# Performance work log

Measured on AMD Instinct MI355X. Metric: run time of the kernel, lower is better.

Reference implementation:

```python
import jax, jax.numpy as jnp
import numpy as np

B, N, F, T, K, C, CT = 64, 307, 64, 12, 3, 64, 64
LN_EPS = 1e-5


def setup_inputs() -> dict:
    key = jax.random.key(0)
    ks = jax.random.split(key, 20)
    s = 0.1  # mild scale so sigmoid/softmax stay in a sane range
    return {
        "x": jax.random.normal(ks[0], (B, N, F, T), jnp.float32),
        "W1": jax.random.normal(ks[1], (T,), jnp.float32) * s,
        "W2": jax.random.normal(ks[2], (F, T), jnp.float32) * s,
        "W3": jax.random.normal(ks[3], (F,), jnp.float32) * s,
        "b_s": jax.random.normal(ks[4], (1, N, N), jnp.float32) * s,
        "V_s": jax.random.normal(ks[5], (N, N), jnp.float32) * s,
        "U1": jax.random.normal(ks[6], (N,), jnp.float32) * s,
        "U2": jax.random.normal(ks[7], (F, N), jnp.float32) * s,
        "U3": jax.random.normal(ks[8], (F,), jnp.float32) * s,
        "b_e": jax.random.normal(ks[9], (1, T, T), jnp.float32) * s,
        "V_e": jax.random.normal(ks[10], (T, T), jnp.float32) * s,
        "cheb": jax.random.normal(ks[11], (K, N, N), jnp.float32) * s,
        "Theta": jax.random.normal(ks[12], (K, F, C), jnp.float32) * s,
        "tconv_w": jax.random.normal(ks[13], (CT, C, 1, 3), jnp.float32) * s,
        "tconv_b": jax.random.normal(ks[14], (CT,), jnp.float32) * s,
        "rconv_w": jax.random.normal(ks[15], (CT, F, 1, 1), jnp.float32) * s,
        "rconv_b": jax.random.normal(ks[16], (CT,), jnp.float32) * s,
        "gamma": jnp.ones((CT,), jnp.float32),
        "beta": jnp.zeros((CT,), jnp.float32),
    }


def _temporal_attention(x, U1, U2, U3, b_e, V_e):
    # x: (B,N,F,T)
    lhs = jnp.einsum('bnft,n->btf', x, U1) @ U2            # (B,T,N)
    rhs = jnp.einsum('f,bnft->bnt', U3, x)                 # (B,N,T)
    prod = jnp.einsum('btn,bns->bts', lhs, rhs)            # (B,T,T)
    E = jnp.einsum('uv,bvt->but', V_e, jax.nn.sigmoid(prod + b_e))
    return jax.nn.softmax(E, axis=1)                       # (B,T,T)


def _spatial_attention(x, W1, W2, W3, b_s, V_s):
    # x: (B,N,F,T)
    lhs = jnp.einsum('bnft,t->bnf', x, W1) @ W2            # (B,N,T)
    rhs = jnp.einsum('f,bnft->btn', W3, x)                 # (B,T,N)
    prod = jnp.einsum('bnt,btm->bnm', lhs, rhs)            # (B,N,N)
    sig = jax.nn.sigmoid(prod + b_s)                       # (B,N,N)
    # torch: (V_s @ sig.T(1,2,0)).T(2,0,1) -> S[b,a,i] = sum_v V_s[i,v]*sig[b,a,v]
    S = jnp.einsum('bav,iv->bai', sig, V_s)
    return jax.nn.softmax(S, axis=1)                       # (B,N,N)


def _cheb_conv_sat(x, S, cheb, Theta):
    # x: (B,N,F,T), S: (B,N,N), cheb: (K,N,N), Theta: (K,F,C)
    A = cheb[:, None] * S[None]                            # (K,B,N,N) attention-masked polys
    # out[b,j,c,t] = sum_{k,i,f} A[k,b,i,j] * x[b,i,f,t] * Theta[k,f,c]
    rhs = jnp.einsum('kbij,bift->kbjft', A, x)             # (K,B,N,F,T)
    out = jnp.einsum('kbjft,kfc->bjct', rhs, Theta)        # (B,N,C,T)
    return jax.nn.relu(out)


def _conv2d(inp, w, b, pad):
    # inp: (B,C_in,N,T), w: (C_out,C_in,kh,kw)
    y = jax.lax.conv_general_dilated(
        inp, w, window_strides=(1, 1), padding=pad,
        dimension_numbers=('NCHW', 'OIHW', 'NCHW'))
    return y + b[None, :, None, None]


def reference(x, W1, W2, W3, b_s, V_s, U1, U2, U3, b_e, V_e,
              cheb, Theta, tconv_w, tconv_b, rconv_w, rconv_b, gamma, beta):
    b, n, f_, t = x.shape
    # temporal attention gating
    E = _temporal_attention(x, U1, U2, U3, b_e, V_e)                      # (B,T,T)
    x_TAt = (x.reshape(b, n * f_, t) @ E).reshape(b, n, f_, t)
    # spatial attention on temporally-gated signal
    S = _spatial_attention(x_TAt, W1, W2, W3, b_s, V_s)                   # (B,N,N)
    # attention-weighted Chebyshev graph conv on original x
    spatial_gcn = _cheb_conv_sat(x, S, cheb, Theta)                       # (B,N,C,T)
    # temporal conv (1,3), SAME padding along time
    tco = _conv2d(spatial_gcn.transpose(0, 2, 1, 3), tconv_w, tconv_b,
                  ((0, 0), (1, 1))).transpose(0, 2, 1, 3)                 # (B,N,CT,T)
    # 1x1 residual conv on x
    res = _conv2d(x.transpose(0, 2, 1, 3), rconv_w, rconv_b,
                  ((0, 0), (0, 0))).transpose(0, 2, 1, 3)                 # (B,N,CT,T)
    h = jax.nn.relu(res + tco)
    # LayerNorm over the filter/channel axis (axis=2)
    mu = jnp.mean(h, axis=2, keepdims=True)
    var = jnp.var(h, axis=2, keepdims=True)
    hn = (h - mu) * jax.lax.rsqrt(var + LN_EPS)
    return hn * gamma[None, None, :, None] + beta[None, None, :, None]
```

## Files before the change

### kernel.cpp

```cpp
#include <hip/hip_runtime.h>
#include <hip/hip_bf16.h>
#include <math.h>

constexpr int B = 64, N = 307, F = 64, T = 12, K = 3, C = 64, CT = 64;
constexpr float LN_EPS = 1e-5f;
constexpr int FT = F * T;

typedef float vf4 __attribute__((ext_vector_type(4)));
typedef short s16x8 __attribute__((ext_vector_type(8)));

__device__ __forceinline__ unsigned short f2bf(float f) {
    unsigned int u = __float_as_uint(f);
    unsigned int r = u + 0x7FFFu + ((u >> 16) & 1u);
    return (unsigned short)(r >> 16);
}


__global__ void k_lhs1_e(const float* __restrict__ x, const float* __restrict__ U1,
                         float* __restrict__ out) {
    int bb = blockIdx.x;
    int b = bb / 3;
    int e = (bb % 3) * 256 + threadIdx.x;
    const float* xp = x + (size_t)b * N * FT + e;
    float s = 0.f;
    for (int n = 0; n < N; n++) s += xp[(size_t)n * FT] * U1[n];
    int f = e / T, t = e % T;
    out[((size_t)b * T + t) * F + f] = s;
}

__global__ void k_xdots(const float* __restrict__ x, const float* __restrict__ U3,
                        const float* __restrict__ W3, float* __restrict__ rhs_e,
                        float* __restrict__ xw3) {
    int idx = blockIdx.x * blockDim.x + threadIdx.x;
    if (idx >= B * N * T) return;
    int t = idx % T;
    size_t bn = idx / T;
    const float* xp = x + bn * F * T + t;
    float s1 = 0.f, s2 = 0.f;
    for (int f = 0; f < F; f++) {
        float v = xp[f * T];
        s1 += U3[f] * v;
        s2 += W3[f] * v;
    }
    rhs_e[idx] = s1;
    xw3[idx] = s2;
}

__global__ void k_lhs_e(const float* __restrict__ lhs1, const float* __restrict__ U2,
                        float* __restrict__ out) {
    int idx = blockIdx.x * blockDim.x + threadIdx.x;
    if (idx >= B * T * N) return;
    int n = idx % N;
    int bt = idx / N;
    const float* lp = lhs1 + (size_t)bt * F;
    float s = 0.f;
    for (int f = 0; f < F; f++) s += lp[f] * U2[f * N + n];
    out[idx] = s;
}

__global__ void k_tatt(const float* __restrict__ lhs, const float* __restrict__ rhs,
                       const float* __restrict__ b_e, const float* __restrict__ V_e,
                       const float* __restrict__ W1, float* __restrict__ E,
                       float* __restrict__ EW1) {
    int b = blockIdx.x;
    int tid = threadIdx.x;
    __shared__ float ll[T][N + 1];
    __shared__ float rr_[T][N + 1];
    __shared__ float sig[T * T];
    __shared__ float Ev[T * T];
    __shared__ float mx[T], sm[T];
    for (int l = tid; l < T * N; l += 256) ll[l / N][l % N] = lhs[(size_t)b * T * N + l];
    for (int l = tid; l < N * T; l += 256) rr_[l % T][l / T] = rhs[(size_t)b * N * T + l];
    __syncthreads();
    if (tid < T * T) {
        int t = tid % T, u = tid / T;
        const vf4* lp4 = (const vf4*)&ll[u][0];
        const vf4* rp4 = (const vf4*)&rr_[t][0];
        float s = 0.f;
#pragma unroll 4
        for (int q = 0; q < 76; q++) {
            vf4 a = lp4[q], c = rp4[q];
            s += a[0] * c[0] + a[1] * c[1] + a[2] * c[2] + a[3] * c[3];
        }
        for (int n = 304; n < N; n++) s += ll[u][n] * rr_[t][n];
        s += b_e[u * T + t];
        sig[tid] = 1.f / (1.f + expf(-s));
    }
    __syncthreads();
    if (tid < T * T) {
        int t = tid % T, u = tid / T;
        float e = 0.f;
        for (int v = 0; v < T; v++) e += V_e[u * T + v] * sig[v * T + t];
        Ev[tid] = e;
    }
    __syncthreads();
    if (tid < T) {
        float m = -1e30f;
        for (int u = 0; u < T; u++) m = fmaxf(m, Ev[u * T + tid]);
        float s = 0.f;
        for (int u = 0; u < T; u++) s += expf(Ev[u * T + tid] - m);
        mx[tid] = m;
        sm[tid] = s;
    }
    __syncthreads();
    if (tid < T * T) {
        int t = tid % T;
        float val = expf(Ev[tid] - mx[t]) / sm[t];
        E[(size_t)b * T * T + tid] = val;
        sig[tid] = val;
    }
    __syncthreads();
    if (tid < T) {
        float s = 0.f;
        for (int t = 0; t < T; t++) s += sig[tid * T + t] * W1[t];
        EW1[(size_t)b * T + tid] = s;
    }
}


__global__ void k_lhs_sf(const float* __restrict__ x, const float* __restrict__ EW1,
                         const float* __restrict__ W2, float* __restrict__ lhs_s) {
    int blk = blockIdx.x;
    int sub = threadIdx.x >> 6;
    int ft = threadIdx.x & 63;
    size_t bn = (size_t)blk * 4 + sub;
    int b = (int)(bn / N);
    __shared__ float a[4][F];
    __shared__ float ew[4][T];
    if (ft < T) ew[sub][ft] = EW1[(size_t)b * T + ft];
    __syncthreads();
    const float* xp = x + bn * FT + ft * T;
    float s = 0.f;
#pragma unroll
    for (int tp = 0; tp < T; tp++) s += xp[tp] * ew[sub][tp];
    a[sub][ft] = s;
    __syncthreads();
    if (ft < T) {
        float s2 = 0.f;
#pragma unroll 8
        for (int f = 0; f < F; f++) s2 += a[sub][f] * W2[f * T + ft];
        lhs_s[bn * T + ft] = s2;
    }
}

__global__ void k_rhs_s2(const float* __restrict__ xw3, const float* __restrict__ E,
                         float* __restrict__ out) {
    int idx = blockIdx.x * blockDim.x + threadIdx.x;
    if (idx >= B * T * N) return;
    int m = idx % N;
    int t = (idx / N) % T;
    int b = idx / (N * T);
    const float* xp = xw3 + ((size_t)b * N + m) * T;
    const float* Ep = E + (size_t)b * T * T + t;
    float s = 0.f;
    for (int tp = 0; tp < T; tp++) s += xp[tp] * Ep[tp * T];
    out[idx] = s;
}

constexpr int PREP_NN = N * N;
constexpr int PREP_TW = CT * C * 3;
constexpr int PREP_TH = K * F * C;
constexpr int PREP_TOT = PREP_NN + PREP_TW + PREP_TH;
constexpr int PREP_CHT = K * N * N;
constexpr int PREP_TOT2 = PREP_TOT + PREP_CHT;

__global__ void k_prep(const float* __restrict__ V, const float* __restrict__ tw,
                       const float* __restrict__ Th, const float* __restrict__ cheb,
                       float* __restrict__ VT, float* __restrict__ twT,
                       float* __restrict__ ThT, float* __restrict__ chebT) {
    int idx = blockIdx.x * blockDim.x + threadIdx.x;
    if (idx < PREP_NN) {
        int v = idx % N;
        int i = idx / N;
        VT[(size_t)v * N + i] = V[(size_t)i * N + v];
    } else if (idx < PREP_NN + PREP_TW) {
        int l = idx - PREP_NN;
        int dt = l % 3;
        int c = (l / 3) % C;
        int ct = l / (3 * C);
        twT[((size_t)dt * CT + ct) * C + c] = tw[l];
    } else if (idx < PREP_TOT) {
        int l = idx - PREP_NN - PREP_TW;
        int c = l % C;
        int f = (l / C) % F;
        int k = l / (C * F);
        ThT[((size_t)k * C + c) * F + f] = Th[l];
    } else if (idx < PREP_TOT2) {
        int l = idx - PREP_TOT;
        int i = l % N;
        int j = (l / N) % N;
        int k = l / (N * N);
        chebT[((size_t)k * N + j) * N + i] = cheb[((size_t)k * N + i) * N + j];
    }
}

constexpr int AT = 4;
constexpr int NAB = (N + AT - 1) / AT;

__global__ void k_sigS(const float* __restrict__ lhs_s, const float* __restrict__ rhs_s,
                       const float* __restrict__ b_s, const float* __restrict__ VsT,
                       float* __restrict__ S) {
    int blk = blockIdx.x;
    int b = blk / NAB;
    int a0 = (blk % NAB) * AT;
    int tid = threadIdx.x;
    __shared__ float lrow[AT][T];
    __shared__ float sig4[AT][N];
    if (tid < AT * T) {
        int a = tid / T, t = tid % T;
        lrow[a][t] = (a0 + a < N) ? lhs_s[((size_t)b * N + a0 + a) * T + t] : 0.f;
    }
    __syncthreads();
    for (int v = tid; v < N; v += 256) {
        float rv[T];
        for (int t = 0; t < T; t++) rv[t] = rhs_s[((size_t)b * T + t) * N + v];
        for (int a = 0; a < AT; a++) {
            if (a0 + a >= N) break;
            float s = 0.f;
            for (int t = 0; t < T; t++) s += lrow[a][t] * rv[t];
            s += b_s[(size_t)(a0 + a) * N + v];
            sig4[a][v] = 1.f / (1.f + expf(-s));
        }
    }
    __syncthreads();
    for (int i = tid; i < N; i += 256) {
        float s[AT] = {0.f, 0.f, 0.f, 0.f};
        for (int v = 0; v < N; v++) {
            float vt = VsT[(size_t)v * N + i];
            for (int a = 0; a < AT; a++) s[a] += sig4[a][v] * vt;
        }
        for (int a = 0; a < AT; a++)
            if (a0 + a < N) S[((size_t)b * N + a0 + a) * N + i] = s[a];
    }
}

__global__ void k_softmax_S(float* __restrict__ S) {
    int idx = blockIdx.x * blockDim.x + threadIdx.x;
    if (idx >= B * N) return;
    int b = idx / N;
    int i = idx % N;
    float* p = S + (size_t)b * N * N + i;
    float m = -1e30f;
    for (int a = 0; a < N; a++) m = fmaxf(m, p[(size_t)a * N]);
    float s = 0.f;
    for (int a = 0; a < N; a++) s += expf(p[(size_t)a * N] - m);
    float inv = 1.f / s;
    for (int a = 0; a < N; a++) p[(size_t)a * N] = expf(p[(size_t)a * N] - m) * inv;
}

__global__ void k_softT(const float* __restrict__ S, float* __restrict__ ST) {
    int b = blockIdx.x >> 1;
    int c0 = (blockIdx.x & 1) * 256;
    int tid = threadIdx.x;
    int c = c0 + tid;
    bool act = c < N;
    const float* p = S + (size_t)b * N * N + c;
    float m = -1e30f, s = 0.f;
    if (act) {
        for (int r = 0; r < N; r++) m = fmaxf(m, p[(size_t)r * N]);
        for (int r = 0; r < N; r++) s += expf(p[(size_t)r * N] - m);
    }
    float inv = act ? 1.f / s : 0.f;
    __shared__ float tile[32][257];
    float* STb = ST + (size_t)b * N * N;
    for (int r0 = 0; r0 < N; r0 += 32) {
        int rmax = min(32, N - r0);
        if (act)
            for (int rr = 0; rr < rmax; rr++)
                tile[rr][tid] = expf(p[(size_t)(r0 + rr) * N] - m) * inv;
        __syncthreads();
        for (int it = 0; it < 32; it++) {
            int cl = 8 * it + (tid >> 5);
            int cc = c0 + cl;
            int r = r0 + (tid & 31);
            if (cc < N && (tid & 31) < rmax) STb[(size_t)cc * N + r] = tile[tid & 31][cl];
        }
        __syncthreads();
    }
}


constexpr int JT = 4;
constexpr int NJB = (N + JT - 1) / JT;
constexpr int GGRID = B * NJB;
constexpr int IP = 320;

constexpr long XI_TOT = (long)B * 48 * 10 * 64;

__global__ void k_xI(const float* __restrict__ x, unsigned short* __restrict__ xI) {
    long idx = (long)blockIdx.x * 256 + threadIdx.x;
    if (idx >= XI_TOT) return;
    int lane = (int)(idx & 63);
    int ks = (int)((idx >> 6) % 10);
    int et = (int)((idx / 640) % 48);
    int b = (int)(idx / 30720);
    int col = lane & 15, kg = lane >> 4;
    int i0 = ks * 32 + kg * 8;
    int e = et * 16 + col;
    const float* xp = x + (size_t)b * N * FT + e;
    s16x8 out;
#pragma unroll
    for (int r = 0; r < 8; r++) {
        int i = i0 + r;
        out[r] = (i < N) ? (short)f2bf(xp[(size_t)i * FT]) : (short)0;
    }
    *(s16x8*)(xI + (size_t)idx * 8) = out;
}

__global__ void k_Wq16(const float* __restrict__ chebT, const float* __restrict__ ST,
                       unsigned short* __restrict__ Wq) {
    long idx = (long)blockIdx.x * 256 + threadIdx.x;
    long tot = (long)B * NJB * 12 * IP;
    if (idx >= tot) return;
    int i = (int)(idx % IP);
    int q = (int)((idx / IP) % 12);
    int jb = (int)((idx / (12L * IP)) % NJB);
    int b = (int)(idx / (12L * IP * NJB));
    int k = q >> 2, jj = q & 3, j = jb * 4 + jj;
    float w = 0.f;
    if (i < N && j < N)
        w = chebT[((size_t)k * N + j) * N + i] * ST[((size_t)b * N + j) * N + i];
    Wq[idx] = f2bf(w);
}

__global__ __launch_bounds__(256, 3) void k_gcnz_m(const unsigned short* __restrict__ xI,
                                                   const unsigned short* __restrict__ WqT,
                                                   const float* __restrict__ ThT,
                                                   float* __restrict__ sg) {
    int blk0 = blockIdx.x;
    int blk = (blk0 & 7) * (GGRID / 8) + (blk0 >> 3);
    int b = blk / NJB;
    int jb = blk % NJB;
    int j0 = jb * JT;
    int tid = threadIdx.x;
    int w = tid >> 6;
    int lane = tid & 63;
    int col = lane & 15;
    int kg = lane >> 4;

    __shared__ float zlf[3 * 3080];

    vf4 acc[12];
#pragma unroll
    for (int mt = 0; mt < 12; mt++) acc[mt] = (vf4){0.f, 0.f, 0.f, 0.f};

    const unsigned short* xb =
        xI + ((size_t)(b * 48 + w * 12) * 10) * 512 + (size_t)lane * 8;
    const unsigned short* wb =
        WqT + ((size_t)(b * NJB + jb) * 12 + (col < 12 ? col : 11)) * IP + kg * 8;

    s16x8 cx[6], nx[6], cw, nw;
    auto ldx = [&](s16x8* d, int h, int ks) {
#pragma unroll
        for (int m = 0; m < 6; m++)
            d[m] = *(const s16x8*)(xb + (size_t)((h * 6 + m) * 10 + ks) * 512);
    };

    cw = *(const s16x8*)(wb);
    ldx(cx, 0, 0);
#pragma unroll
    for (int step = 0; step < 20; step++) {
        int ks = step >> 1, h = step & 1;
        if (step < 19) {
            int ns = step + 1;
            int nks = ns >> 1, nh = ns & 1;
            nw = (nh == 0) ? *(const s16x8*)(wb + nks * 32) : cw;
            ldx(nx, nh, nks);
        }
#pragma unroll
        for (int m = 0; m < 6; m++)
            acc[h * 6 + m] =
                __builtin_amdgcn_mfma_f32_16x16x32_bf16(cw, cx[m], acc[h * 6 + m], 0, 0, 0);
        if (step < 19) {
            cw = nw;
#pragma unroll
            for (int m = 0; m < 6; m++) cx[m] = nx[m];
        }
        (void)ks;
    }

    if (kg < 3) {
#pragma unroll
        for (int mt = 0; mt < 12; mt++) {
            int e = w * 192 + mt * 16 + col;
            *(vf4*)(zlf + kg * 3080 + e * 4) = acc[mt];
        }
    }
    __syncthreads();

    if (tid < 192) {
        int t = tid % T;
        int c0 = (tid / T) * 4;
        float s[4][4];
#pragma unroll
        for (int cc = 0; cc < 4; cc++)
#pragma unroll
            for (int jj = 0; jj < 4; jj++) s[cc][jj] = 0.f;

#pragma unroll
        for (int k = 0; k < K; k++) {
            const vf4* zpk = (const vf4*)(zlf + k * 3080 + t * 4);
            const vf4* tp0 = (const vf4*)(ThT + ((size_t)k * C + c0 + 0) * F);
            const vf4* tp1 = (const vf4*)(ThT + ((size_t)k * C + c0 + 1) * F);
            const vf4* tp2 = (const vf4*)(ThT + ((size_t)k * C + c0 + 2) * F);
            const vf4* tp3 = (const vf4*)(ThT + ((size_t)k * C + c0 + 3) * F);
#pragma unroll 4
            for (int fq = 0; fq < F / 4; fq++) {
                vf4 z0 = zpk[(4 * fq + 0) * 12];
                vf4 z1 = zpk[(4 * fq + 1) * 12];
                vf4 z2 = zpk[(4 * fq + 2) * 12];
                vf4 z3 = zpk[(4 * fq + 3) * 12];
                vf4 th[4];
                th[0] = tp0[fq];
                th[1] = tp1[fq];
                th[2] = tp2[fq];
                th[3] = tp3[fq];
#pragma unroll
                for (int cc = 0; cc < 4; cc++) {
#pragma unroll
                    for (int jj = 0; jj < 4; jj++)
                        s[cc][jj] += th[cc][0] * z0[jj] + th[cc][1] * z1[jj] +
                                     th[cc][2] * z2[jj] + th[cc][3] * z3[jj];
                }
            }
        }
#pragma unroll
        for (int jj = 0; jj < 4; jj++) {
            int j = j0 + jj;
            if (j < N) {
                float* op = sg + ((size_t)b * N + j) * FT + (size_t)c0 * T + t;
                op[0 * T] = fmaxf(s[0][jj], 0.f);
                op[1 * T] = fmaxf(s[1][jj], 0.f);
                op[2 * T] = fmaxf(s[2][jj], 0.f);
                op[3 * T] = fmaxf(s[3][jj], 0.f);
            }
        }
    }
}


__global__ void k_Wp(const float* __restrict__ cheb, const float* __restrict__ S,
                     float* __restrict__ Wp) {
    long idx = (long)blockIdx.x * 256 + threadIdx.x;
    long tot = (long)B * NJB * N * 12;
    if (idx >= tot) return;
    int q = (int)(idx % 12);
    int i = (int)((idx / 12) % N);
    int jb = (int)((idx / (12L * N)) % NJB);
    int b = (int)(idx / (12L * N * NJB));
    int k = q >> 2, jj = q & 3;
    int j = jb * 4 + jj;
    float w = 0.f;
    if (j < N) w = cheb[((size_t)k * N + i) * N + j] * S[((size_t)b * N + i) * N + j];
    Wp[idx] = w;
}

__global__ __launch_bounds__(256, 4) void k_gcnz_p(const float* __restrict__ x,
                                                   const float* __restrict__ Wp,
                                                   const float* __restrict__ ThT,
                                                   float* __restrict__ sg) {
    int blk0 = blockIdx.x;
    int blk = (blk0 & 7) * (GGRID / 8) + (blk0 >> 3);
    int b = blk / NJB;
    int jb = blk % NJB;
    int j0 = jb * JT;
    int tid = threadIdx.x;

    __shared__ float zl[K][F][T][JT];

    float acc[K * JT][3];
#pragma unroll
    for (int m = 0; m < K * JT; m++)
#pragma unroll
        for (int r = 0; r < 3; r++) acc[m][r] = 0.f;

    const float* xp = x + (size_t)b * N * FT + 3 * tid;
    const float* wb = Wp + ((size_t)b * NJB + jb) * N * 12;

    float w0[12], w1[12], w2[12];
    float x0[3], x1[3], x2[3];

    auto LD = [&](float* wreg, float* xreg, int i) {
        const vf4* p = (const vf4*)(wb + (size_t)i * 12);
        vf4 a = p[0], b4 = p[1], c4 = p[2];
#pragma unroll
        for (int q = 0; q < 4; q++) {
            wreg[q] = a[q];
            wreg[4 + q] = b4[q];
            wreg[8 + q] = c4[q];
        }
        const float* xq = xp + (size_t)i * FT;
        xreg[0] = xq[0];
        xreg[1] = xq[1];
        xreg[2] = xq[2];
    };
    auto FMA = [&](const float* wreg, const float* xreg) {
#pragma unroll
        for (int m = 0; m < K * JT; m++) {
            acc[m][0] += wreg[m] * xreg[0];
            acc[m][1] += wreg[m] * xreg[1];
            acc[m][2] += wreg[m] * xreg[2];
        }
    };

    LD(w0, x0, 0);
    LD(w1, x1, 1);
    LD(w2, x2, 2);
    int i = 0;
    for (; i + 5 < N; i += 3) {
        float a0[12], a1[12], a2[12], y0[3], y1[3], y2[3];
        LD(a0, y0, i + 3);
        LD(a1, y1, i + 4);
        LD(a2, y2, i + 5);
        FMA(w0, x0);
        FMA(w1, x1);
        FMA(w2, x2);
#pragma unroll
        for (int m = 0; m < 12; m++) {
            w0[m] = a0[m];
            w1[m] = a1[m];
            w2[m] = a2[m];
        }
#pragma unroll
        for (int r = 0; r < 3; r++) {
            x0[r] = y0[r];
            x1[r] = y1[r];
            x2[r] = y2[r];
        }
    }
    FMA(w0, x0);
    FMA(w1, x1);
    FMA(w2, x2);
    for (i += 3; i < N; i++) {
        LD(w0, x0, i);
        FMA(w0, x0);
    }

#pragma unroll
    for (int r = 0; r < 3; r++) {
        int e = 3 * tid + r;
        int f = e / T, t = e % T;
#pragma unroll
        for (int m = 0; m < K * JT; m++) zl[m >> 2][f][t][m & 3] = acc[m][r];
    }
    __syncthreads();

    if (tid < 192) {
        int t = tid % T;
        int c0 = (tid / T) * 4;
        float s[4][4];
#pragma unroll
        for (int cc = 0; cc < 4; cc++)
#pragma unroll
            for (int jj = 0; jj < 4; jj++) s[cc][jj] = 0.f;

#pragma unroll
        for (int k = 0; k < K; k++) {
            const vf4* zpk = (const vf4*)&zl[k][0][t][0];
            const vf4* tp0 = (const vf4*)(ThT + ((size_t)k * C + c0 + 0) * F);
            const vf4* tp1 = (const vf4*)(ThT + ((size_t)k * C + c0 + 1) * F);
            const vf4* tp2 = (const vf4*)(ThT + ((size_t)k * C + c0 + 2) * F);
            const vf4* tp3 = (const vf4*)(ThT + ((size_t)k * C + c0 + 3) * F);
#pragma unroll 4
            for (int fq = 0; fq < F / 4; fq++) {
                vf4 z0 = zpk[(4 * fq + 0) * 12];
                vf4 z1 = zpk[(4 * fq + 1) * 12];
                vf4 z2 = zpk[(4 * fq + 2) * 12];
                vf4 z3 = zpk[(4 * fq + 3) * 12];
                vf4 th[4];
                th[0] = tp0[fq];
                th[1] = tp1[fq];
                th[2] = tp2[fq];
                th[3] = tp3[fq];
#pragma unroll
                for (int cc = 0; cc < 4; cc++) {
#pragma unroll
                    for (int jj = 0; jj < 4; jj++)
                        s[cc][jj] += th[cc][0] * z0[jj] + th[cc][1] * z1[jj] +
                                     th[cc][2] * z2[jj] + th[cc][3] * z3[jj];
                }
            }
        }
#pragma unroll
        for (int jj = 0; jj < 4; jj++) {
            int j = j0 + jj;
            if (j < N) {
                float* op = sg + ((size_t)b * N + j) * FT + (size_t)c0 * T + t;
                op[0 * T] = fmaxf(s[0][jj], 0.f);
                op[1 * T] = fmaxf(s[1][jj], 0.f);
                op[2 * T] = fmaxf(s[2][jj], 0.f);
                op[3 * T] = fmaxf(s[3][jj], 0.f);
            }
        }
    }
}


constexpr int RB = 4;
constexpr int PF = 68;

__global__ void k_rest(const float* __restrict__ x, const float* __restrict__ twT,
                       const float* __restrict__ tb, const float* __restrict__ rw,
                       const float* __restrict__ rb, const float* __restrict__ gamma,
                       const float* __restrict__ beta, float* __restrict__ io) {
    int blk = blockIdx.x;
    size_t bn0 = (size_t)blk * RB;
    int tid = threadIdx.x;

    __shared__ float xt[RB][T][PF];
    __shared__ float sgt[RB][T + 2][PF];
    __shared__ float red0[RB][T][17];
    __shared__ float red1[RB][T][17];
    __shared__ float mus[RB][T], rstds[RB][T];

    for (int l = tid; l < RB * PF; l += 192) {
        int rr = l / PF, c = l % PF;
        sgt[rr][0][c] = 0.f;
        sgt[rr][T + 1][c] = 0.f;
    }
    for (int l = tid; l < RB * FT; l += 192) {
        int rr = l / FT, rem = l % FT;
        int f = rem / T, t = rem % T;
        xt[rr][t][f] = x[(bn0 + rr) * FT + rem];
        sgt[rr][t + 1][f] = io[(bn0 + rr) * FT + rem];
    }
    __syncthreads();

    int t = tid % T;
    int cg = tid / T;
    int ct0 = cg * 4;

    float acc[RB][4];
#pragma unroll
    for (int rr = 0; rr < RB; rr++)
#pragma unroll
        for (int q = 0; q < 4; q++) acc[rr][q] = rb[ct0 + q] + tb[ct0 + q];

    {
        const vf4* w0 = (const vf4*)(rw + (size_t)(ct0 + 0) * F);
        const vf4* w1 = (const vf4*)(rw + (size_t)(ct0 + 1) * F);
        const vf4* w2 = (const vf4*)(rw + (size_t)(ct0 + 2) * F);
        const vf4* w3 = (const vf4*)(rw + (size_t)(ct0 + 3) * F);
#pragma unroll 4
        for (int fq = 0; fq < F / 4; fq++) {
            vf4 a = w0[fq], b4 = w1[fq], c4 = w2[fq], d4 = w3[fq];
#pragma unroll
            for (int rr = 0; rr < RB; rr++) {
                vf4 v = *(const vf4*)(&xt[rr][t][fq * 4]);
                acc[rr][0] += a[0] * v[0] + a[1] * v[1] + a[2] * v[2] + a[3] * v[3];
                acc[rr][1] += b4[0] * v[0] + b4[1] * v[1] + b4[2] * v[2] + b4[3] * v[3];
                acc[rr][2] += c4[0] * v[0] + c4[1] * v[1] + c4[2] * v[2] + c4[3] * v[3];
                acc[rr][3] += d4[0] * v[0] + d4[1] * v[1] + d4[2] * v[2] + d4[3] * v[3];
            }
        }
    }
#pragma unroll
    for (int dt = 0; dt < 3; dt++) {
        const vf4* w0 = (const vf4*)(twT + ((size_t)dt * CT + ct0 + 0) * C);
        const vf4* w1 = (const vf4*)(twT + ((size_t)dt * CT + ct0 + 1) * C);
        const vf4* w2 = (const vf4*)(twT + ((size_t)dt * CT + ct0 + 2) * C);
        const vf4* w3 = (const vf4*)(twT + ((size_t)dt * CT + ct0 + 3) * C);
#pragma unroll 4
        for (int fq = 0; fq < C / 4; fq++) {
            vf4 a = w0[fq], b4 = w1[fq], c4 = w2[fq], d4 = w3[fq];
#pragma unroll
            for (int rr = 0; rr < RB; rr++) {
                vf4 v = *(const vf4*)(&sgt[rr][t + dt][fq * 4]);
                acc[rr][0] += a[0] * v[0] + a[1] * v[1] + a[2] * v[2] + a[3] * v[3];
                acc[rr][1] += b4[0] * v[0] + b4[1] * v[1] + b4[2] * v[2] + b4[3] * v[3];
                acc[rr][2] += c4[0] * v[0] + c4[1] * v[1] + c4[2] * v[2] + c4[3] * v[3];
                acc[rr][3] += d4[0] * v[0] + d4[1] * v[1] + d4[2] * v[2] + d4[3] * v[3];
            }
        }
    }

#pragma unroll
    for (int rr = 0; rr < RB; rr++) {
        float ps = 0.f;
#pragma unroll
        for (int q = 0; q < 4; q++) {
            float h = fmaxf(acc[rr][q], 0.f);
            acc[rr][q] = h;
            ps += h;
        }
        red0[rr][t][cg] = ps;
    }
    __syncthreads();
    if (tid < RB * T) {
        int rr = tid / T, tt = tid % T;
        float m = 0.f;
#pragma unroll 4
        for (int g = 0; g < 16; g++) m += red0[rr][tt][g];
        mus[rr][tt] = m * (1.f / CT);
    }
    __syncthreads();
#pragma unroll
    for (int rr = 0; rr < RB; rr++) {
        float m = mus[rr][t];
        float pv = 0.f;
#pragma unroll
        for (int q = 0; q < 4; q++) {
            float d = acc[rr][q] - m;
            pv += d * d;
        }
        red1[rr][t][cg] = pv;
    }
    __syncthreads();
    if (tid < RB * T) {
        int rr = tid / T, tt = tid % T;
        float v = 0.f;
#pragma unroll 4
        for (int g = 0; g < 16; g++) v += red1[rr][tt][g];
        rstds[rr][tt] = rsqrtf(v * (1.f / CT) + LN_EPS);
    }
    __syncthreads();
#pragma unroll
    for (int rr = 0; rr < RB; rr++) {
        float m = mus[rr][t], rs = rstds[rr][t];
        float* iop = io + (bn0 + rr) * FT;
#pragma unroll
        for (int q = 0; q < 4; q++) {
            int ct = ct0 + q;
            iop[ct * T + t] = (acc[rr][q] - m) * rs * gamma[ct] + beta[ct];
        }
    }
}


extern "C" void kernel_launch(void* const* d_in, const int* in_sizes, int n_in,
                              void* d_out, int out_size, void* d_ws, size_t ws_size,
                              hipStream_t stream) {
    const float* x     = (const float*)d_in[0];
    const float* W1    = (const float*)d_in[1];
    const float* W2    = (const float*)d_in[2];
    const float* W3    = (const float*)d_in[3];
    const float* b_s   = (const float*)d_in[4];
    const float* V_s   = (const float*)d_in[5];
    const float* U1    = (const float*)d_in[6];
    const float* U2    = (const float*)d_in[7];
    const float* U3    = (const float*)d_in[8];
    const float* b_e   = (const float*)d_in[9];
    const float* V_e   = (const float*)d_in[10];
    const float* cheb  = (const float*)d_in[11];
    const float* Theta = (const float*)d_in[12];
    const float* tw    = (const float*)d_in[13];
    const float* tb    = (const float*)d_in[14];
    const float* rw    = (const float*)d_in[15];
    const float* rb    = (const float*)d_in[16];
    const float* gam   = (const float*)d_in[17];
    const float* bet   = (const float*)d_in[18];
    float* out = (float*)d_out;

    float* ws = (float*)d_ws;
    size_t off = 0;
    auto alloc = [&](size_t n) { float* p = ws + off; off += n; return p; };
    float* VsT = alloc((size_t)N * N);
    float* twT = alloc((size_t)CT * C * 3);
    float* ThT = alloc((size_t)K * F * C);
    size_t base_end = off;
    float* lhs1_e = alloc((size_t)B * T * F);
    float* lhs_e  = alloc((size_t)B * T * N);
    float* rhs_e  = alloc((size_t)B * N * T);
    float* Ebuf   = alloc((size_t)B * T * T);
    float* EW1    = alloc((size_t)B * T);
    float* xw3    = alloc((size_t)B * N * T);
    float* lhs_s  = alloc((size_t)B * N * T);
    float* rhs_s  = alloc((size_t)B * T * N);
    float* Sb     = alloc((size_t)B * N * N);
    size_t poolA_end = off;

    size_t wq_fl = (size_t)B * NJB * 12 * IP / 2;
    unsigned short* WqT = (unsigned short*)(ws + base_end);
    size_t off2 = base_end + wq_fl;
    if (off2 < poolA_end) off2 = poolA_end;
    float* chebT = ws + off2; off2 += (size_t)K * N * N;
    float* SbT = ws + off2; off2 += (size_t)B * N * N;
    unsigned short* xI = (unsigned short*)(ws + off2);
    off2 += (size_t)XI_TOT * 8 / 2;
    bool useM = ws_size >= off2 * sizeof(float);

    size_t wp_off = (poolA_end + 3) & ~(size_t)3;
    float* Wp = ws + wp_off;
    bool useWp = !useM && ws_size >= (wp_off + (size_t)B * NJB * N * 12) * sizeof(float);

    auto g = [](long n) { return dim3((unsigned)((n + 255) / 256)); };

    k_prep<<<g(useM ? (long)PREP_TOT2 : (long)PREP_TOT), 256, 0, stream>>>(
        V_s, tw, Theta, cheb, VsT, twT, ThT, chebT);
    if (useM) k_xI<<<g(XI_TOT), 256, 0, stream>>>(x, xI);

    k_lhs1_e<<<dim3(B * 3), 256, 0, stream>>>(x, U1, lhs1_e);
    k_xdots<<<g((long)B * N * T), 256, 0, stream>>>(x, U3, W3, rhs_e, xw3);
    k_lhs_e<<<g((long)B * T * N), 256, 0, stream>>>(lhs1_e, U2, lhs_e);
    k_tatt<<<B, 256, 0, stream>>>(lhs_e, rhs_e, b_e, V_e, W1, Ebuf, EW1);

    k_lhs_sf<<<dim3((B * N) / 4), 256, 0, stream>>>(x, EW1, W2, lhs_s);
    k_rhs_s2<<<g((long)B * T * N), 256, 0, stream>>>(xw3, Ebuf, rhs_s);
    k_sigS<<<B * NAB, 256, 0, stream>>>(lhs_s, rhs_s, b_s, VsT, Sb);

    if (useM) {
        k_softT<<<dim3(B * 2), 256, 0, stream>>>(Sb, SbT);
        k_Wq16<<<g((long)B * NJB * 12 * IP), 256, 0, stream>>>(chebT, SbT, WqT);
        k_gcnz_m<<<GGRID, 256, 0, stream>>>(xI, WqT, ThT, out);
    } else if (useWp) {
        k_softmax_S<<<g((long)B * N), 256, 0, stream>>>(Sb);
        k_Wp<<<g((long)B * NJB * N * 12), 256, 0, stream>>>(cheb, Sb, Wp);
        k_gcnz_p<<<GGRID, 256, 0, stream>>>(x, Wp, ThT, out);
    }

    k_rest<<<(B * N) / RB, 192, 0, stream>>>(x, twT, tb, rw, rb, gam, bet, out);
}
```

Baseline: 919.4 us.

## Double-buffer full k-step loads in gcn MFMA kernel and widen sigS row tile

Measured after the change: 952.3 us. 3.6% more time.

```diff
diff --git a/kernel.cpp b/kernel.cpp
--- a/kernel.cpp
+++ b/kernel.cpp
@@ -194,7 +194,7 @@
     }
 }
 
-constexpr int AT = 4;
+constexpr int AT = 8;
 constexpr int NAB = (N + AT - 1) / AT;
 
 __global__ void k_sigS(const float* __restrict__ lhs_s, const float* __restrict__ rhs_s,
@@ -224,11 +224,15 @@
     }
     __syncthreads();
     for (int i = tid; i < N; i += 256) {
-        float s[AT] = {0.f, 0.f, 0.f, 0.f};
+        float s[AT];
+#pragma unroll
+        for (int a = 0; a < AT; a++) s[a] = 0.f;
         for (int v = 0; v < N; v++) {
             float vt = VsT[(size_t)v * N + i];
+#pragma unroll
             for (int a = 0; a < AT; a++) s[a] += sig4[a][v] * vt;
         }
+#pragma unroll
         for (int a = 0; a < AT; a++)
             if (a0 + a < N) S[((size_t)b * N + a0 + a) * N + i] = s[a];
     }
@@ -323,7 +327,7 @@
     Wq[idx] = f2bf(w);
 }
 
-__global__ __launch_bounds__(256, 3) void k_gcnz_m(const unsigned short* __restrict__ xI,
+__global__ __launch_bounds__(256, 2) void k_gcnz_m(const unsigned short* __restrict__ xI,
                                                    const unsigned short* __restrict__ WqT,
                                                    const float* __restrict__ ThT,
                                                    float* __restrict__ sg) {
@@ -349,34 +353,26 @@
     const unsigned short* wb =
         WqT + ((size_t)(b * NJB + jb) * 12 + (col < 12 ? col : 11)) * IP + kg * 8;
 
-    s16x8 cx[6], nx[6], cw, nw;
-    auto ldx = [&](s16x8* d, int h, int ks) {
-#pragma unroll
-        for (int m = 0; m < 6; m++)
-            d[m] = *(const s16x8*)(xb + (size_t)((h * 6 + m) * 10 + ks) * 512);
+    s16x8 xa[12], xc[12], wa, wc;
+    auto ldg = [&](s16x8* d, s16x8& wreg, int ks) {
+        wreg = *(const s16x8*)(wb + ks * 32);
+#pragma unroll
+        for (int m = 0; m < 12; m++)
+            d[m] = *(const s16x8*)(xb + (size_t)(m * 10 + ks) * 512);
     };
-
-    cw = *(const s16x8*)(wb);
-    ldx(cx, 0, 0);
-#pragma unroll
-    for (int step = 0; step < 20; step++) {
-        int ks = step >> 1, h = step & 1;
-        if (step < 19) {
-            int ns = step + 1;
-            int nks = ns >> 1, nh = ns & 1;
-            nw = (nh == 0) ? *(const s16x8*)(wb + nks * 32) : cw;
-            ldx(nx, nh, nks);
-        }
-#pragma unroll
-        for (int m = 0; m < 6; m++)
-            acc[h * 6 + m] =
-                __builtin_amdgcn_mfma_f32_16x16x32_bf16(cw, cx[m], acc[h * 6 + m], 0, 0, 0);
-        if (step < 19) {
-            cw = nw;
-#pragma unroll
-            for (int m = 0; m < 6; m++) cx[m] = nx[m];
-        }
-        (void)ks;
+    auto mma = [&](const s16x8* d, s16x8 wreg) {
+#pragma unroll
+        for (int m = 0; m < 12; m++)
+            acc[m] = __builtin_amdgcn_mfma_f32_16x16x32_bf16(wreg, d[m], acc[m], 0, 0, 0);
+    };
+
+    ldg(xa, wa, 0);
+#pragma unroll
+    for (int ks2 = 0; ks2 < 5; ks2++) {
+        ldg(xc, wc, 2 * ks2 + 1);
+        mma(xa, wa);
+        if (ks2 < 4) ldg(xa, wa, 2 * ks2 + 2);
+        mma(xc, wc);
     }
 
     if (kg < 3) {
```
